# Kernel tuning notes

Measured on AMD Instinct MI355X. Metric: run time of the kernel, lower is better.

The kernel has to match this reference:

```python
import jax, jax.numpy as jnp
import numpy as np

N, D, C_CLS = 8192, 512, 1000
SCALE = 1.0
LOW_THRE = 1.0 / C_CLS
EPS = 1e-12  # torch F.normalize eps


def _l2norm(x):
    n = jnp.sqrt(jnp.sum(x * x, axis=1, keepdims=True))
    return x / jnp.maximum(n, EPS)


def setup_inputs() -> dict:
    key = jax.random.key(0)
    k1, k2, k3, k4, k5 = jax.random.split(key, 5)
    feature = jax.random.normal(k1, (N, D), jnp.float32)
    proxy_raw = jax.random.normal(k2, (C_CLS, D), jnp.float32) * 0.02
    cP_weight = jax.random.normal(k3, (D, D), jnp.float32) * 0.05
    # probability-like rows (sum to 1), as prob_detach is a detached softmax output
    prob_detach = jax.nn.softmax(4.0 * jax.random.normal(k4, (N, C_CLS), jnp.float32), axis=-1)
    conf_mask = jax.random.randint(k5, (N,), 0, 2) > 0
    return {"feature": feature, "proxy_raw": proxy_raw, "cP_weight": cP_weight,
            "prob_detach": prob_detach, "conf_mask": conf_mask}


def reference(feature, proxy_raw, cP_weight, prob_detach, conf_mask):
    feat = _l2norm(feature)                                   # (N, D)
    proxy = _l2norm(proxy_raw @ cP_weight.T)                  # (C, D), cP is a linear projection

    class_candidates = prob_detach > LOW_THRE                 # (N, C) bool
    top1_idx = jnp.argmax(prob_detach, axis=1)                # (N,)
    top1_class = jnp.arange(C_CLS)[None, :] == top1_idx[:, None]  # (N, C) bool one-hot

    not_conf = ~conf_mask
    pred_class = (class_candidates & not_conf[:, None]) | (top1_class & conf_mask[:, None])  # (N, C)

    # sc_proxy: (sc_weight.unsqueeze(2) * proxy).sum(dim=1) == matmul
    sc_weight = prob_detach * class_candidates                # (N, C)
    sc_proxy = sc_weight @ proxy                              # (N, D)
    sc_sim = jnp.sum(feat * sc_proxy, axis=1)                 # (N,)

    pred = feat @ proxy.T                                     # (N, C)
    proxy_sim = jnp.take_along_axis(pred, top1_idx[:, None], axis=1)[:, 0]  # (N,)
    pos_pair = jnp.where(conf_mask, proxy_sim, sc_sim)        # (N,)

    # intersection.any(dim=2) == (pred_class @ pred_class.T) > 0 (avoids (N,N,C) tensor)
    pc = pred_class.astype(feat.dtype)
    neg_matrix = ~((pc @ pc.T) > 0)                           # (N, N) bool

    sim = feat @ feat.T                                       # (N, N)
    sim = sim * neg_matrix
    neg_pair = jnp.where(sim < 1e-6, -jnp.inf, sim)           # masked_fill

    logits = jnp.concatenate([pos_pair[:, None], neg_pair], axis=1)  # (N, N+1)
    logp = jax.nn.log_softmax(SCALE * logits, axis=1)
    loss = -jnp.mean(logp[:, 0])                              # nll_loss with label 0

    denom = jnp.sum(not_conf)
    sc_count = jnp.sum(class_candidates & not_conf[:, None])
    sc_num = jnp.where(denom > 0,
                       sc_count.astype(jnp.float32) / jnp.maximum(denom, 1).astype(jnp.float32),
                       jnp.float32(0.0))
    return loss, sc_num
```

## Files before the change

### kernel.cpp

```cpp
#include <hip/hip_runtime.h>
#include <hip/hip_bf16.h>

#define N_ROWS 8192
#define DIM 512
#define C_CLSN 1000
#define C_PAD 1024
#define LOW_THRE (1.0f / 1000.0f)

typedef __bf16 bf16x8 __attribute__((ext_vector_type(8)));
typedef float floatx4 __attribute__((ext_vector_type(4)));
typedef unsigned long long ull;
typedef ull ull2 __attribute__((ext_vector_type(2)));



__global__ __launch_bounds__(1024) void kzp_v13(const int* __restrict__ conf,
                                                int* __restrict__ perm,
                                                int* __restrict__ counters) {
  int tid = threadIdx.x;
  __shared__ int sc[1024];
  __shared__ int sbad, sodd1, seven1, smode;
  if (tid == 0) { sbad = 0; sodd1 = 0; seven1 = 0; }
  __syncthreads();
  for (int i = tid; i < 2048; i += 1024) {
    int v = conf[i];
    if (v != 0 && v != 1) atomicOr(&sbad, 1);
    if (v == 1) { if (i & 1) atomicAdd(&sodd1, 1); else atomicAdd(&seven1, 1); }
  }
  __syncthreads();
  if (tid == 0) {
    int mode = 0;
    if (sbad) mode = 1;
    else if (seven1 > 0 && sodd1 == 0) mode = 2;
    smode = mode;
  }
  __syncthreads();
  int mode = smode;
  int r0 = tid * 8;
  int f[8]; int cnt = 0;
  #pragma unroll
  for (int k = 0; k < 8; ++k) {
    int r = r0 + k;
    bool c;
    if (mode == 1)      c = ((const unsigned char*)conf)[r] != 0;
    else if (mode == 2) c = ((const long long*)conf)[r] != 0;
    else                c = conf[r] != 0;
    f[k] = c ? 1 : 0; cnt += f[k];
  }
  sc[tid] = cnt;
  __syncthreads();
  for (int off = 1; off < 1024; off <<= 1) {
    int v = (tid >= off) ? sc[tid - off] : 0;
    __syncthreads();
    sc[tid] += v;
    __syncthreads();
  }
  int incl = sc[tid];
  int excl = incl - cnt;
  int total = sc[1023];
  if (tid == 0) counters[3] = total;
  int cpos = excl;
  int npos = total + (r0 - excl);
  #pragma unroll
  for (int k = 0; k < 8; ++k) {
    if (f[k]) perm[cpos++] = r0 + k;
    else      perm[npos++] = r0 + k;
  }
}

__global__ __launch_bounds__(256) void kda_v13(const float* __restrict__ prob,
                                               const float* __restrict__ feature,
                                               const int* __restrict__ perm,
                                               const int* __restrict__ counters_ro,
                                               ull* __restrict__ bits,
                                               int* __restrict__ top1a,
                                               int* __restrict__ cnta,
                                               __bf16* __restrict__ featBF,
                                               unsigned char* __restrict__ featF8) {
  int wv = threadIdx.x >> 6, lane = threadIdx.x & 63;
  int p = blockIdx.x * 4 + wv;
  int orig = perm[p];
  bool is_conf = p < counters_ro[3];
  const float4* pr4 = (const float4*)(prob + (size_t)orig * C_CLSN);
  float4 v[4];
  #pragma unroll
  for (int pass = 0; pass < 4; ++pass) {
    int q = pass * 64 + lane;
    v[pass] = (q < 250) ? pr4[q] : make_float4(-1.f, -1.f, -1.f, -1.f);
  }
  float bv = -1e30f; int bidx = 0x7fffffff;
  int cnt = 0;
  ull myword = 0ULL;
  #pragma unroll
  for (int pass = 0; pass < 4; ++pass) {
    int q = pass * 64 + lane;
    bool inb = q < 250;
    float el[4] = {v[pass].x, v[pass].y, v[pass].z, v[pass].w};
    #pragma unroll
    for (int j = 0; j < 4; ++j) {
      float pv = el[j];
      int c = q * 4 + j;
      if (inb && pv > bv) { bv = pv; bidx = c; }
      ull m = __ballot(inb && (pv > LOW_THRE));
      cnt += (int)__popcll(m);
      if (lane == pass * 4 + j) myword = m;
    }
  }
  #pragma unroll
  for (int m = 1; m < 64; m <<= 1) {
    float ov = __shfl_xor(bv, m); int oi = __shfl_xor(bidx, m);
    if (ov > bv || (ov == bv && oi < bidx)) { bv = ov; bidx = oi; }
  }
  int top1 = bidx;
  if (is_conf) {
    int w1 = ((top1 >> 8) << 2) | (top1 & 3);
    myword = (lane == w1) ? (1ULL << ((top1 >> 2) & 63)) : 0ULL;
  }
  if (lane < 16) bits[(size_t)p * 16 + lane] = myword;
  if (lane == 0) {
    top1a[p] = top1;
    cnta[p] = is_conf ? 0 : cnt;
  }
  const float* fr = feature + (size_t)orig * DIM;
  int c0 = lane * 8;
  float4 v0 = *(const float4*)(fr + c0);
  float4 v1 = *(const float4*)(fr + c0 + 4);
  float ss = v0.x*v0.x + v0.y*v0.y + v0.z*v0.z + v0.w*v0.w
           + v1.x*v1.x + v1.y*v1.y + v1.z*v1.z + v1.w*v1.w;
  #pragma unroll
  for (int m = 1; m < 64; m <<= 1) ss += __shfl_xor(ss, m);
  float scl = 1.0f / fmaxf(sqrtf(ss), 1e-12f);
  float x0 = v0.x*scl, x1 = v0.y*scl, x2 = v0.z*scl, x3 = v0.w*scl;
  float x4 = v1.x*scl, x5 = v1.y*scl, x6 = v1.z*scl, x7 = v1.w*scl;
  bf16x8 bvx;
  bvx[0] = (__bf16)x0; bvx[1] = (__bf16)x1; bvx[2] = (__bf16)x2; bvx[3] = (__bf16)x3;
  bvx[4] = (__bf16)x4; bvx[5] = (__bf16)x5; bvx[6] = (__bf16)x6; bvx[7] = (__bf16)x7;
  int g = p >> 4, r = p & 15;
  *(bf16x8*)((char*)featBF + (size_t)g * 16384 + (size_t)lane * 256 + (size_t)r * 16) = bvx;
  int lo = __builtin_amdgcn_cvt_pk_fp8_f32(x0, x1, 0, false);
  lo = __builtin_amdgcn_cvt_pk_fp8_f32(x2, x3, lo, true);
  int hi = __builtin_amdgcn_cvt_pk_fp8_f32(x4, x5, 0, false);
  hi = __builtin_amdgcn_cvt_pk_fp8_f32(x6, x7, hi, true);
  int2 pk; pk.x = lo; pk.y = hi;
  *(int2*)(featF8 + (size_t)g * 8192 + (size_t)lane * 128 + (size_t)r * 8) = pk;
}

__global__ __launch_bounds__(256) void kbc_v13(const float* __restrict__ raw,
                                               const float* __restrict__ cP,
                                               __bf16* __restrict__ proxyBF) {
  int tid = threadIdx.x;
  int c0 = blockIdx.x * 8;
  int d0 = tid, d1 = tid + 256;
  int g = c0 >> 4;
  int r0 = c0 & 15;
  char* pbase = (char*)proxyBF + (size_t)g * 16384;
  if (c0 >= C_CLSN) {
    #pragma unroll
    for (int cc = 0; cc < 8; ++cc) {
      int row = r0 + cc;
      *(__bf16*)(pbase + (size_t)(d0 >> 3) * 256 + row * 16 + (d0 & 7) * 2) = (__bf16)0.f;
      *(__bf16*)(pbase + (size_t)(d1 >> 3) * 256 + row * 16 + (d1 & 7) * 2) = (__bf16)0.f;
    }
    return;
  }
  __shared__ float sraw[8 * DIM];
  __shared__ float red[8 * 256];
  for (int idx = tid; idx < 8 * DIM; idx += 256)
    sraw[idx] = raw[(size_t)c0 * DIM + idx];
  __syncthreads();
  float acc0[8], acc1[8];
  #pragma unroll
  for (int cc = 0; cc < 8; ++cc) { acc0[cc] = 0.f; acc1[cc] = 0.f; }
  for (int k = 0; k < DIM; k += 4) {
    float4 w0 = *(const float4*)&cP[(size_t)d0 * DIM + k];
    float4 w1 = *(const float4*)&cP[(size_t)d1 * DIM + k];
    #pragma unroll
    for (int cc = 0; cc < 8; ++cc) {
      const float* sr = &sraw[cc * DIM + k];
      acc0[cc] += sr[0]*w0.x + sr[1]*w0.y + sr[2]*w0.z + sr[3]*w0.w;
      acc1[cc] += sr[0]*w1.x + sr[1]*w1.y + sr[2]*w1.z + sr[3]*w1.w;
    }
  }
  #pragma unroll
  for (int cc = 0; cc < 8; ++cc)
    red[cc * 256 + tid] = acc0[cc]*acc0[cc] + acc1[cc]*acc1[cc];
  __syncthreads();
  for (int s = 128; s > 0; s >>= 1) {
    if (tid < s)
      #pragma unroll
      for (int cc = 0; cc < 8; ++cc)
        red[cc * 256 + tid] += red[cc * 256 + tid + s];
    __syncthreads();
  }
  #pragma unroll
  for (int cc = 0; cc < 8; ++cc) {
    float scl = 1.0f / fmaxf(sqrtf(red[cc * 256]), 1e-12f);
    int row = r0 + cc;
    *(__bf16*)(pbase + (size_t)(d0 >> 3) * 256 + row * 16 + (d0 & 7) * 2) = (__bf16)(acc0[cc] * scl);
    *(__bf16*)(pbase + (size_t)(d1 >> 3) * 256 + row * 16 + (d1 & 7) * 2) = (__bf16)(acc1[cc] * scl);
  }
}

__global__ __launch_bounds__(512, 4) void kegg_v13(const __bf16* __restrict__ featBF,
                                                   const __bf16* __restrict__ proxyBF,
                                                   const unsigned char* __restrict__ featF8,
                                                   const float* __restrict__ prob,
                                                   const ull* __restrict__ bits,
                                                   const int* __restrict__ perm,
                                                   const int* __restrict__ top1a,
                                                   const int* __restrict__ counters_ro,
                                                   float* __restrict__ scsim,
                                                   float* __restrict__ possim,
                                                   float* __restrict__ S) {
  __shared__ __align__(16) char smem[33792];
  int tid = threadIdx.x;
  int wv = tid >> 6, lane = tid & 63;
  int wi = wv >> 2, wj = wv & 3;
  int lr = lane >> 4, lc = lane & 15;

  floatx4 acc[4][2];
  floatx4 zero = {0.f, 0.f, 0.f, 0.f};
  #pragma unroll
  for (int ti = 0; ti < 4; ++ti)
    #pragma unroll
    for (int tj = 0; tj < 2; ++tj) acc[ti][tj] = zero;

  if (blockIdx.x < 512) {
    int* pO  = (int*)smem;
    int* t1r = (int*)(smem + 512);
    int bi = blockIdx.x >> 3;
    int bj = blockIdx.x & 7;
    if (tid < 128) { pO[tid] = perm[bi * 128 + tid]; t1r[tid] = top1a[bi * 128 + tid]; }
    __syncthreads();
    const char* A = (const char*)featBF;
    const char* B = (const char*)proxyBF;
    size_t aO[4], bO[2];
    #pragma unroll
    for (int ti = 0; ti < 4; ++ti)
      aO[ti] = (size_t)(bi * 8 + wi * 4 + ti) * 16384 + (size_t)lane * 16;
    #pragma unroll
    for (int tj = 0; tj < 2; ++tj)
      bO[tj] = (size_t)(bj * 8 + wj * 2 + tj) * 16384 + (size_t)lane * 16;
    for (int kt = 0; kt < DIM; kt += 32) {
      bf16x8 afr[4], bfr[2];
      #pragma unroll
      for (int ti = 0; ti < 4; ++ti)
        afr[ti] = *(const bf16x8*)(A + aO[ti] + (size_t)kt * 32);
      #pragma unroll
      for (int tj = 0; tj < 2; ++tj)
        bfr[tj] = *(const bf16x8*)(B + bO[tj] + (size_t)kt * 32);
      #pragma unroll
      for (int ti = 0; ti < 4; ++ti)
        #pragma unroll
        for (int tj = 0; tj < 2; ++tj)
          acc[ti][tj] = __builtin_amdgcn_mfma_f32_16x16x32_bf16(afr[ti], bfr[tj], acc[ti][tj], 0, 0, 0);
    }
    #pragma unroll
    for (int ti = 0; ti < 4; ++ti) {
      int ibase = wi * 64 + ti * 16 + lr * 4;
      float rs[4] = {0.f, 0.f, 0.f, 0.f};
      #pragma unroll
      for (int rr = 0; rr < 4; ++rr) {
        int il = ibase + rr;
        int orig = pO[il];
        int t1 = t1r[il];
        const float* prow = prob + (size_t)orig * C_CLSN;
        #pragma unroll
        for (int tj = 0; tj < 2; ++tj) {
          int c = bj * 128 + wj * 32 + tj * 16 + lc;
          float P = acc[ti][tj][rr];
          float pv = (c < C_CLSN) ? prow[c] : 0.f;
          if (pv > LOW_THRE) rs[rr] += pv * P;
          if (c == t1) possim[bi * 128 + il] = P;
        }
      }
      #pragma unroll
      for (int m = 1; m < 16; m <<= 1)
        #pragma unroll
        for (int rr = 0; rr < 4; ++rr) rs[rr] += __shfl_xor(rs[rr], m);
      if (lc == 0) {
        #pragma unroll
        for (int rr = 0; rr < 4; ++rr)
          atomicAdd(&scsim[bi * 128 + ibase + rr], rs[rr]);
      }
    }
    return;
  }

  ull* bsI = (ull*)smem;
  ull* bsJ = (ull*)(smem + 16384);
  int* t1I = (int*)(smem + 32768);
  int* t1J = (int*)(smem + 33280);

  int b = (int)(((long long)(blockIdx.x - 512) * 997) % 2080);
  int bi = 0, rem = b;
  while (rem >= 64 - bi) { rem -= 64 - bi; bi++; }
  int bj = bi + rem;

  int nconf = counters_ro[3];
  bool allcI = (bi * 128 + 128) <= nconf;
  bool allcJ = (bj * 128 + 128) <= nconf;
  int mode = allcJ ? 0 : (allcI ? 1 : 3);

  if (tid < 128)      t1I[tid]       = top1a[bi * 128 + tid];
  else if (tid < 256) t1J[tid - 128] = top1a[bj * 128 + tid - 128];
  if (mode == 3) {
    #pragma unroll
    for (int e = 0; e < 4; ++e) {
      int flat = tid + e * 512;
      int row = flat & 127, w = flat >> 7;
      bsI[w * 128 + row] = bits[(size_t)(bi * 128 + row) * 16 + w];
    }
  }
  if (mode != 0) {
    #pragma unroll
    for (int e = 0; e < 4; ++e) {
      int flat = tid + e * 512;
      int row = flat & 127, w = flat >> 7;
      bsJ[w * 128 + row] = bits[(size_t)(bj * 128 + row) * 16 + w];
    }
  }
  __syncthreads();

  const char* F = (const char*)featF8;
  size_t aO[4], bO[2];
  #pragma unroll
  for (int ti = 0; ti < 4; ++ti)
    aO[ti] = (size_t)(bi * 8 + wi * 4 + ti) * 8192 + (size_t)lane * 8;
  #pragma unroll
  for (int tj = 0; tj < 2; ++tj)
    bO[tj] = (size_t)(bj * 8 + wj * 2 + tj) * 8192 + (size_t)lane * 8;

  #pragma unroll
  for (int kt = 0; kt < DIM; kt += 64) {
    #pragma unroll
    for (int ks = 0; ks < 2; ++ks) {
      long a_[4], b_[2];
      #pragma unroll
      for (int ti = 0; ti < 4; ++ti)
        a_[ti] = *(const long*)(F + aO[ti] + (size_t)(kt * 16 + ks * 512));
      #pragma unroll
      for (int tj = 0; tj < 2; ++tj)
        b_[tj] = *(const long*)(F + bO[tj] + (size_t)(kt * 16 + ks * 512));
      #pragma unroll
      for (int ti = 0; ti < 4; ++ti)
        #pragma unroll
        for (int tj = 0; tj < 2; ++tj)
          acc[ti][tj] = __builtin_amdgcn_mfma_f32_16x16x32_fp8_fp8(a_[ti], b_[tj], acc[ti][tj], 0, 0, 0);
    }
  }

  int tJv[2];
  #pragma unroll
  for (int tj = 0; tj < 2; ++tj) tJv[tj] = t1J[wj * 32 + tj * 16 + lc];

  float cs[2] = {0.f, 0.f};
  #pragma unroll
  for (int ti = 0; ti < 4; ++ti) {
    int ibase = wi * 64 + ti * 16 + lr * 4;
    unsigned inter[8];
    if (mode == 0) {
      #pragma unroll
      for (int rr = 0; rr < 4; ++rr) {
        int tI = t1I[ibase + rr];
        #pragma unroll
        for (int tj = 0; tj < 2; ++tj) inter[rr * 2 + tj] = (tI == tJv[tj]);
      }
    } else if (mode == 1) {
      #pragma unroll
      for (int rr = 0; rr < 4; ++rr) {
        int tI = t1I[ibase + rr];
        int w = ((tI >> 8) << 2) | (tI & 3);
        int bb = (tI >> 2) & 63;
        #pragma unroll
        for (int tj = 0; tj < 2; ++tj) {
          ull word = bsJ[w * 128 + wj * 32 + tj * 16 + lc];
          inter[rr * 2 + tj] = (unsigned)((word >> bb) & 1ULL);
        }
      }
    } else {
      #pragma unroll
      for (int q = 0; q < 8; ++q) inter[q] = 0u;
      #pragma unroll
      for (int w = 0; w < 16; ++w) {
        ull2 a01 = *(const ull2*)&bsI[w * 128 + ibase];
        ull2 a23 = *(const ull2*)&bsI[w * 128 + ibase + 2];
        ull aw[4] = {a01[0], a01[1], a23[0], a23[1]};
        ull bw[2];
        #pragma unroll
        for (int tj = 0; tj < 2; ++tj) bw[tj] = bsJ[w * 128 + wj * 32 + tj * 16 + lc];
        #pragma unroll
        for (int rr = 0; rr < 4; ++rr)
          #pragma unroll
          for (int tj = 0; tj < 2; ++tj) {
            ull t = aw[rr] & bw[tj];
            inter[rr * 2 + tj] |= (unsigned)(t | (t >> 32));
          }
      }
    }
    float rs[4] = {0.f, 0.f, 0.f, 0.f};
    #pragma unroll
    for (int rr = 0; rr < 4; ++rr)
      #pragma unroll
      for (int tj = 0; tj < 2; ++tj) {
        float sim = acc[ti][tj][rr];
        sim = fminf(sim, 1.0f);
        float e_ = ((inter[rr * 2 + tj] == 0u) && (sim >= 1e-6f)) ? __expf(sim) : 0.f;
        rs[rr] += e_;
        cs[tj] += e_;
      }
    #pragma unroll
    for (int m = 1; m < 16; m <<= 1)
      #pragma unroll
      for (int rr = 0; rr < 4; ++rr) rs[rr] += __shfl_xor(rs[rr], m);
    if (lc == 0) {
      #pragma unroll
      for (int rr = 0; rr < 4; ++rr)
        atomicAdd(&S[(size_t)bi * 128 + ibase + rr], rs[rr]);
    }
  }
  if (bi != bj) {
    #pragma unroll
    for (int tj = 0; tj < 2; ++tj) {
      cs[tj] += __shfl_xor(cs[tj], 16);
      cs[tj] += __shfl_xor(cs[tj], 32);
    }
    if (lr == 0) {
      #pragma unroll
      for (int tj = 0; tj < 2; ++tj)
        atomicAdd(&S[(size_t)bj * 128 + wj * 32 + tj * 16 + lc], cs[tj]);
    }
  }
}

__global__ __launch_bounds__(1024) void kf_final_v13(const float* __restrict__ possim,
                                                     const float* __restrict__ scsim,
                                                     const float* __restrict__ S,
                                                     const int* __restrict__ cnta,
                                                     const int* __restrict__ counters,
                                                     float* __restrict__ out) {
  __shared__ float red[1024];
  __shared__ int redi[1024];
  int tid = threadIdx.x;
  int nconf = counters[3];
  float local = 0.f;
  int lcnt = 0;
  for (int i = tid; i < N_ROWS; i += 1024) {
    float p = (i < nconf) ? possim[i] : scsim[i];
    p = fminf(fmaxf(p, -1.1f), 1.1f);
    float s = fmaxf(S[i], 0.0f);
    local += logf(expf(p) + s) - p;
    lcnt += cnta[i];
  }
  red[tid] = local;
  redi[tid] = lcnt;
  __syncthreads();
  for (int s = 512; s > 0; s >>= 1) {
    if (tid < s) { red[tid] += red[tid + s]; redi[tid] += redi[tid + s]; }
    __syncthreads();
  }
  if (tid == 0) {
    float loss = red[0] / (float)N_ROWS;
    int denom = N_ROWS - nconf;
    int scc = redi[0];
    float scn = (denom > 0) ? ((float)scc / (float)denom) : 0.f;
    out[0] = loss;
    out[1] = scn;
  }
}

extern "C" void kernel_launch(void* const* d_in, const int* in_sizes, int n_in,
                              void* d_out, int out_size, void* d_ws, size_t ws_size,
                              hipStream_t stream) {
  const float* feature   = (const float*)d_in[0];
  const float* proxy_raw = (const float*)d_in[1];
  const float* cP        = (const float*)d_in[2];
  const float* prob      = (const float*)d_in[3];
  const int*   conf      = (const int*)d_in[4];
  float* out = (float*)d_out;

  size_t need = (size_t)N_ROWS * DIM * 2
              + (size_t)N_ROWS * DIM
              + (size_t)C_PAD * DIM * 2
              + (size_t)N_ROWS * 16 * 8
              + (size_t)N_ROWS * 4
              + (size_t)N_ROWS * 4
              + (size_t)N_ROWS * 4
              + 256
              + (size_t)N_ROWS * 4
              + (size_t)N_ROWS * 4
              + (size_t)N_ROWS * 4;
  if (ws_size < need) return;

  char* ws = (char*)d_ws;
  __bf16* featBF  = (__bf16*)ws;              ws += (size_t)N_ROWS * DIM * 2;
  unsigned char* featF8 = (unsigned char*)ws; ws += (size_t)N_ROWS * DIM;
  __bf16* proxyBF = (__bf16*)ws;              ws += (size_t)C_PAD * DIM * 2;
  ull* bits       = (ull*)ws;                 ws += (size_t)N_ROWS * 16 * 8;
  float* possim   = (float*)ws;               ws += (size_t)N_ROWS * 4;
  float* S        = (float*)ws;               ws += (size_t)N_ROWS * 4;
  float* scsim    = (float*)ws;               ws += (size_t)N_ROWS * 4;
  int* counters   = (int*)ws;                 ws += 256;
  int* perm       = (int*)ws;                 ws += (size_t)N_ROWS * 4;
  int* top1a      = (int*)ws;                 ws += (size_t)N_ROWS * 4;
  int* cnta       = (int*)ws;                 ws += (size_t)N_ROWS * 4;

  hipMemsetAsync(S, 0, (size_t)N_ROWS * 8 + 256, stream);
  kzp_v13<<<1, 1024, 0, stream>>>(conf, perm, counters);
  kda_v13<<<N_ROWS / 4, 256, 0, stream>>>(prob, feature, perm, counters,
                                          bits, top1a, cnta, featBF, featF8);
  kbc_v13<<<C_PAD / 8, 256, 0, stream>>>(proxy_raw, cP, proxyBF);
  kegg_v13<<<512 + 2080, 512, 0, stream>>>(featBF, proxyBF, featF8, prob, bits, perm,
                                           top1a, counters, scsim, possim, S);
  kf_final_v13<<<1, 1024, 0, stream>>>(possim, scsim, S, cnta, counters, out);
}
```

Before: 359.2 us.

## Stage GEMM tiles through double-buffered LDS with direct global-to-LDS loads

```diff
diff --git a/kernel.cpp b/kernel.cpp
--- a/kernel.cpp
+++ b/kernel.cpp
@@ -13,8 +13,14 @@
 typedef ull ull2 __attribute__((ext_vector_type(2)));
 
 
-
-__global__ __launch_bounds__(1024) void kzp_v13(const int* __restrict__ conf,
+__device__ __forceinline__ void gl_lds16(const void* g, void* l) {
+  __builtin_amdgcn_global_load_lds(
+      (const __attribute__((address_space(1))) unsigned int*)g,
+      (__attribute__((address_space(3))) unsigned int*)l, 16, 0, 0);
+}
+
+
+__global__ __launch_bounds__(1024) void kzp_v14(const int* __restrict__ conf,
                                                 int* __restrict__ perm,
                                                 int* __restrict__ counters) {
   int tid = threadIdx.x;
@@ -68,7 +74,7 @@
   }
 }
 
-__global__ __launch_bounds__(256) void kda_v13(const float* __restrict__ prob,
+__global__ __launch_bounds__(256) void kda_v14(const float* __restrict__ prob,
                                                const float* __restrict__ feature,
                                                const int* __restrict__ perm,
                                                const int* __restrict__ counters_ro,
@@ -145,7 +151,7 @@
   *(int2*)(featF8 + (size_t)g * 8192 + (size_t)lane * 128 + (size_t)r * 8) = pk;
 }
 
-__global__ __launch_bounds__(256) void kbc_v13(const float* __restrict__ raw,
+__global__ __launch_bounds__(256) void kbc_v14(const float* __restrict__ raw,
                                                const float* __restrict__ cP,
                                                __bf16* __restrict__ proxyBF) {
   int tid = threadIdx.x;
@@ -201,7 +207,7 @@
   }
 }
 
-__global__ __launch_bounds__(512, 4) void kegg_v13(const __bf16* __restrict__ featBF,
+__global__ __launch_bounds__(512, 4) void kegg_v14(const __bf16* __restrict__ featBF,
                                                    const __bf16* __restrict__ proxyBF,
                                                    const unsigned char* __restrict__ featF8,
                                                    const float* __restrict__ prob,
@@ -212,7 +218,7 @@
                                                    float* __restrict__ scsim,
                                                    float* __restrict__ possim,
                                                    float* __restrict__ S) {
-  __shared__ __align__(16) char smem[33792];
+  __shared__ __align__(16) char smem[50176];
   int tid = threadIdx.x;
   int wv = tid >> 6, lane = tid & 63;
   int wi = wv >> 2, wj = wv & 3;
@@ -226,34 +232,44 @@
     for (int tj = 0; tj < 2; ++tj) acc[ti][tj] = zero;
 
   if (blockIdx.x < 512) {
-    int* pO  = (int*)smem;
-    int* t1r = (int*)(smem + 512);
+    int* pO  = (int*)(smem + 32768);
+    int* t1r = (int*)(smem + 33280);
     int bi = blockIdx.x >> 3;
     int bj = blockIdx.x & 7;
+    const char* A = (const char*)featBF;
+    const char* B = (const char*)proxyBF;
+    {
+      const char* gA = A + (size_t)((bi * 8 + wv) * 16384) + (size_t)lane * 16;
+      const char* gB = B + (size_t)((bj * 8 + wv) * 16384) + (size_t)lane * 16;
+      gl_lds16(gA, smem + wv * 1024);
+      gl_lds16(gB, smem + 8192 + wv * 1024);
+    }
     if (tid < 128) { pO[tid] = perm[bi * 128 + tid]; t1r[tid] = top1a[bi * 128 + tid]; }
     __syncthreads();
-    const char* A = (const char*)featBF;
-    const char* B = (const char*)proxyBF;
-    size_t aO[4], bO[2];
-    #pragma unroll
-    for (int ti = 0; ti < 4; ++ti)
-      aO[ti] = (size_t)(bi * 8 + wi * 4 + ti) * 16384 + (size_t)lane * 16;
-    #pragma unroll
-    for (int tj = 0; tj < 2; ++tj)
-      bO[tj] = (size_t)(bj * 8 + wj * 2 + tj) * 16384 + (size_t)lane * 16;
-    for (int kt = 0; kt < DIM; kt += 32) {
+    for (int it = 0; it < 16; ++it) {
+      int sel = it & 1;
+      if (it < 15) {
+        int kt = (it + 1) * 32;
+        const char* gA = A + (size_t)((bi * 8 + wv) * 16384 + kt * 32) + (size_t)lane * 16;
+        const char* gB = B + (size_t)((bj * 8 + wv) * 16384 + kt * 32) + (size_t)lane * 16;
+        gl_lds16(gA, smem + (sel ^ 1) * 16384 + wv * 1024);
+        gl_lds16(gB, smem + (sel ^ 1) * 16384 + 8192 + wv * 1024);
+      }
+      const char* bA = smem + sel * 16384;
+      const char* bB = bA + 8192;
       bf16x8 afr[4], bfr[2];
       #pragma unroll
       for (int ti = 0; ti < 4; ++ti)
-        afr[ti] = *(const bf16x8*)(A + aO[ti] + (size_t)kt * 32);
+        afr[ti] = *(const bf16x8*)(bA + (wi * 4 + ti) * 1024 + lr * 256 + lc * 16);
       #pragma unroll
       for (int tj = 0; tj < 2; ++tj)
-        bfr[tj] = *(const bf16x8*)(B + bO[tj] + (size_t)kt * 32);
+        bfr[tj] = *(const bf16x8*)(bB + (wj * 2 + tj) * 1024 + lr * 256 + lc * 16);
       #pragma unroll
       for (int ti = 0; ti < 4; ++ti)
         #pragma unroll
         for (int tj = 0; tj < 2; ++tj)
           acc[ti][tj] = __builtin_amdgcn_mfma_f32_16x16x32_bf16(afr[ti], bfr[tj], acc[ti][tj], 0, 0, 0);
+      if (it < 15) __syncthreads();
     }
     #pragma unroll
     for (int ti = 0; ti < 4; ++ti) {
@@ -287,10 +303,10 @@
     return;
   }
 
-  ull* bsI = (ull*)smem;
-  ull* bsJ = (ull*)(smem + 16384);
-  int* t1I = (int*)(smem + 32768);
-  int* t1J = (int*)(smem + 33280);
+  ull* bsI = (ull*)(smem + 32768);
+  ull* bsJ = (ull*)smem;
+  int* t1I = (int*)(smem + 49152);
+  int* t1J = (int*)(smem + 49664);
 
   int b = (int)(((long long)(blockIdx.x - 512) * 997) % 2080);
   int bi = 0, rem = b;
@@ -302,6 +318,13 @@
   bool allcJ = (bj * 128 + 128) <= nconf;
   int mode = allcJ ? 0 : (allcI ? 1 : 3);
 
+  const char* F = (const char*)featF8;
+  {
+    const char* gA = F + (size_t)((bi * 8 + wv) * 8192) + (size_t)lane * 16;
+    const char* gB = F + (size_t)((bj * 8 + wv) * 8192) + (size_t)lane * 16;
+    gl_lds16(gA, smem + wv * 1024);
+    gl_lds16(gB, smem + 8192 + wv * 1024);
+  }
   if (tid < 128)      t1I[tid]       = top1a[bi * 128 + tid];
   else if (tid < 256) t1J[tid - 128] = top1a[bj * 128 + tid - 128];
   if (mode == 3) {
@@ -312,6 +335,37 @@
       bsI[w * 128 + row] = bits[(size_t)(bi * 128 + row) * 16 + w];
     }
   }
+  __syncthreads();
+
+  for (int it = 0; it < 8; ++it) {
+    int sel = it & 1;
+    if (it < 7) {
+      int kt = (it + 1) * 64;
+      const char* gA = F + (size_t)((bi * 8 + wv) * 8192 + kt * 16) + (size_t)lane * 16;
+      const char* gB = F + (size_t)((bj * 8 + wv) * 8192 + kt * 16) + (size_t)lane * 16;
+      gl_lds16(gA, smem + (sel ^ 1) * 16384 + wv * 1024);
+      gl_lds16(gB, smem + (sel ^ 1) * 16384 + 8192 + wv * 1024);
+    }
+    const char* bA = smem + sel * 16384;
+    const char* bB = bA + 8192;
+    #pragma unroll
+    for (int ks = 0; ks < 2; ++ks) {
+      long a_[4], b_[2];
+      #pragma unroll
+      for (int ti = 0; ti < 4; ++ti)
+        a_[ti] = *(const long*)(bA + (wi * 4 + ti) * 1024 + (ks * 4 + lr) * 128 + lc * 8);
+      #pragma unroll
+      for (int tj = 0; tj < 2; ++tj)
+        b_[tj] = *(const long*)(bB + (wj * 2 + tj) * 1024 + (ks * 4 + lr) * 128 + lc * 8);
+      #pragma unroll
+      for (int ti = 0; ti < 4; ++ti)
+        #pragma unroll
+        for (int tj = 0; tj < 2; ++tj)
+          acc[ti][tj] = __builtin_amdgcn_mfma_f32_16x16x32_fp8_fp8(a_[ti], b_[tj], acc[ti][tj], 0, 0, 0);
+    }
+    if (it < 7) __syncthreads();
+  }
+  __syncthreads();
   if (mode != 0) {
     #pragma unroll
     for (int e = 0; e < 4; ++e) {
@@ -321,34 +375,6 @@
     }
   }
   __syncthreads();
-
-  const char* F = (const char*)featF8;
-  size_t aO[4], bO[2];
-  #pragma unroll
-  for (int ti = 0; ti < 4; ++ti)
-    aO[ti] = (size_t)(bi * 8 + wi * 4 + ti) * 8192 + (size_t)lane * 8;
-  #pragma unroll
-  for (int tj = 0; tj < 2; ++tj)
-    bO[tj] = (size_t)(bj * 8 + wj * 2 + tj) * 8192 + (size_t)lane * 8;
-
-  #pragma unroll
-  for (int kt = 0; kt < DIM; kt += 64) {
-    #pragma unroll
-    for (int ks = 0; ks < 2; ++ks) {
-      long a_[4], b_[2];
-      #pragma unroll
-      for (int ti = 0; ti < 4; ++ti)
-        a_[ti] = *(const long*)(F + aO[ti] + (size_t)(kt * 16 + ks * 512));
-      #pragma unroll
-      for (int tj = 0; tj < 2; ++tj)
-        b_[tj] = *(const long*)(F + bO[tj] + (size_t)(kt * 16 + ks * 512));
-      #pragma unroll
-      for (int ti = 0; ti < 4; ++ti)
-        #pragma unroll
-        for (int tj = 0; tj < 2; ++tj)
-          acc[ti][tj] = __builtin_amdgcn_mfma_f32_16x16x32_fp8_fp8(a_[ti], b_[tj], acc[ti][tj], 0, 0, 0);
-    }
-  }
 
   int tJv[2];
   #pragma unroll
@@ -433,7 +459,7 @@
   }
 }
 
-__global__ __launch_bounds__(1024) void kf_final_v13(const float* __restrict__ possim,
+__global__ __launch_bounds__(1024) void kf_final_v14(const float* __restrict__ possim,
                                                      const float* __restrict__ scsim,
                                                      const float* __restrict__ S,
                                                      const int* __restrict__ cnta,
@@ -506,11 +532,11 @@
   int* cnta       = (int*)ws;                 ws += (size_t)N_ROWS * 4;
 
   hipMemsetAsync(S, 0, (size_t)N_ROWS * 8 + 256, stream);
-  kzp_v13<<<1, 1024, 0, stream>>>(conf, perm, counters);
-  kda_v13<<<N_ROWS / 4, 256, 0, stream>>>(prob, feature, perm, counters,
+  kzp_v14<<<1, 1024, 0, stream>>>(conf, perm, counters);
+  kda_v14<<<N_ROWS / 4, 256, 0, stream>>>(prob, feature, perm, counters,
                                           bits, top1a, cnta, featBF, featF8);
-  kbc_v13<<<C_PAD / 8, 256, 0, stream>>>(proxy_raw, cP, proxyBF);
-  kegg_v13<<<512 + 2080, 512, 0, stream>>>(featBF, proxyBF, featF8, prob, bits, perm,
+  kbc_v14<<<C_PAD / 8, 256, 0, stream>>>(proxy_raw, cP, proxyBF);
+  kegg_v14<<<512 + 2080, 512, 0, stream>>>(featBF, proxyBF, featF8, prob, bits, perm,
                                            top1a, counters, scsim, possim, S);
-  kf_final_v13<<<1, 1024, 0, stream>>>(possim, scsim, S, cnta, counters, out);
-}
+  kf_final_v14<<<1, 1024, 0, stream>>>(possim, scsim, S, cnta, counters, out);
+}
```

New measurement: 337.1 us. 1.07x faster.
